# Kernel optimization log

Hardware: AMD Instinct MI355X
Metric: run time of the kernel (lower is better)

## Reference

```python
import jax, jax.numpy as jnp
import numpy as np

NEG_INF_DIAG = 1000000.0

def setup_inputs() -> dict:
    key = jax.random.key(0)
    k1, k2, k3 = jax.random.split(key, 3)
    B, N, S, D = 64, 32, 256, 128
    return {
        "query_embeddings": jax.random.normal(k1, (B, N, D), dtype=jnp.float32),
        "doc_embeddings": jax.random.normal(k2, (B, S, D), dtype=jnp.float32),
        "neg_doc_embeddings": jax.random.normal(k3, (B, S, D), dtype=jnp.float32),
    }

def _maxsim(q, d):
    # q: (b, n, dim), d: (b, s, dim) -> (b,) sum over n of max over s of q.d
    return jnp.einsum('bnd,bsd->bns', q, d).max(axis=2).sum(axis=1)

def reference(query_embeddings, doc_embeddings, neg_doc_embeddings):
    pos_scores = _maxsim(query_embeddings, doc_embeddings)
    neg_scores = _maxsim(query_embeddings, neg_doc_embeddings)
    loss = jax.nn.softplus(neg_scores - pos_scores).mean()

    # in-batch term: scores[b, c] = MaxSim(query b, doc c)
    scores = jnp.einsum('bnd,csd->bcns', query_embeddings, doc_embeddings).max(axis=3).sum(axis=2)  # (B, B)
    pos = jnp.diagonal(scores)
    B = scores.shape[0]
    neg = (scores - jnp.eye(B, dtype=scores.dtype) * NEG_INF_DIAG).max(axis=1)
    loss = loss + jax.nn.softplus(neg - pos).mean()
    return loss / 2
```

## Files before the change

kernel.cpp:

```cpp
#include <hip/hip_runtime.h>
#include <hip/hip_bf16.h>

#define B_SZ 64
#define N_Q 32

typedef __attribute__((ext_vector_type(8))) short bf16x8;
typedef __attribute__((ext_vector_type(4))) float f32x4;

static __device__ __forceinline__ unsigned short f2bf(float f) {
    __hip_bfloat16 h = __float2bfloat16(f);
    return *reinterpret_cast<unsigned short*>(&h);
}

static __device__ __forceinline__ bf16x8 cvt_frag(const float* __restrict__ src) {
    float4 a = reinterpret_cast<const float4*>(src)[0];
    float4 b = reinterpret_cast<const float4*>(src)[1];
    union { bf16x8 v; unsigned short u[8]; } t;
    t.u[0] = f2bf(a.x); t.u[1] = f2bf(a.y); t.u[2] = f2bf(a.z); t.u[3] = f2bf(a.w);
    t.u[4] = f2bf(b.x); t.u[5] = f2bf(b.y); t.u[6] = f2bf(b.z); t.u[7] = f2bf(b.w);
    return t.v;
}

#define MFMA(A, Bv, C) __builtin_amdgcn_mfma_f32_16x16x32_bf16(A, Bv, C, 0, 0, 0)

__global__ __launch_bounds__(256) void cvt_permute(const float* __restrict__ q,
                                                   const float* __restrict__ dd,
                                                   const float* __restrict__ nd,
                                                   unsigned short* __restrict__ DP,
                                                   unsigned short* __restrict__ QP) {
    const int blk = blockIdx.x, tid = threadIdx.x;
    if (blk < 2048) {
        const int o = blk * 256 + tid;
        const int doc = o >> 12;
        const int u = o & 4095;
        const int ln = u & 63, nt = (u >> 6) & 3, kk = (u >> 8) & 3, w = u >> 10;
        const int s  = w * 64 + nt * 16 + (ln & 15);
        const int k0 = kk * 32 + (ln >> 4) * 8;
        const float* src = ((doc < 64) ? (dd + (size_t)doc * 32768)
                                       : (nd + (size_t)(doc - 64) * 32768)) + s * 128 + k0;
        reinterpret_cast<bf16x8*>(DP)[o] = cvt_frag(src);
    } else {
        const int g = (blk - 2048) * 256 + tid;
        const int b = g >> 9, u = g & 511;
        const int ln = u & 63, mt = (u >> 6) & 1, kk = u >> 7;
        const int n  = mt * 16 + (ln & 15);
        const int k0 = kk * 32 + (ln >> 4) * 8;
        reinterpret_cast<bf16x8*>(QP)[g] = cvt_frag(q + (size_t)b * 4096 + n * 128 + k0);
    }
}

__global__ __launch_bounds__(256, 2) void maxsim_kernel(const unsigned short* __restrict__ QP,
                                                        const unsigned short* __restrict__ DP,
                                                        float* __restrict__ scores) {
    const int idx = blockIdx.x;
    int b0, nb, ccol, dcc;
    if (idx < 1024) {
        dcc = idx >> 4; b0 = (idx & 15) * 4; nb = 4; ccol = dcc;
    } else {
        b0 = idx - 1024; nb = 1; ccol = B_SZ; dcc = B_SZ + b0;
    }

    const int tid = threadIdx.x;
    const int wave = tid >> 6, lane = tid & 63;
    const int l15 = lane & 15, l4 = lane >> 4;

    __shared__ bf16x8 docB[4][16][64];
    __shared__ float wred[4][4][N_Q];

    const bf16x8* dsrc = reinterpret_cast<const bf16x8*>(DP)
                         + (size_t)dcc * 4096 + wave * 1024 + lane;
    #pragma unroll
    for (int f = 0; f < 16; ++f)
        docB[wave][f][lane] = dsrc[f * 64];

    const bf16x8* QP8 = reinterpret_cast<const bf16x8*>(QP);

    const int npairs = (nb + 1) >> 1;
    for (int g = 0; g < npairs; ++g) {
        const int bb0 = 2 * g;
        const int bb1 = (2 * g + 1 < nb) ? 2 * g + 1 : 2 * g;
        const bf16x8* qA = QP8 + (size_t)(b0 + bb0) * 512 + lane;
        const bf16x8* qB = QP8 + (size_t)(b0 + bb1) * 512 + lane;

        f32x4 acc[2][2][4] = {};
        #pragma unroll
        for (int kk = 0; kk < 4; ++kk) {
            bf16x8 aA0 = qA[kk * 128];
            bf16x8 aA1 = qA[kk * 128 + 64];
            bf16x8 aB0 = qB[kk * 128];
            bf16x8 aB1 = qB[kk * 128 + 64];
            #pragma unroll
            for (int nt = 0; nt < 4; ++nt) {
                bf16x8 Bv = docB[wave][kk * 4 + nt][lane];
                acc[0][0][nt] = MFMA(aA0, Bv, acc[0][0][nt]);
                acc[0][1][nt] = MFMA(aA1, Bv, acc[0][1][nt]);
                acc[1][0][nt] = MFMA(aB0, Bv, acc[1][0][nt]);
                acc[1][1][nt] = MFMA(aB1, Bv, acc[1][1][nt]);
            }
        }

        #pragma unroll
        for (int h = 0; h < 2; ++h) {
            const int bb = (h == 0) ? bb0 : bb1;
            #pragma unroll
            for (int mt = 0; mt < 2; ++mt) {
                #pragma unroll
                for (int reg = 0; reg < 4; ++reg) {
                    float m = fmaxf(fmaxf(acc[h][mt][0][reg], acc[h][mt][1][reg]),
                                    fmaxf(acc[h][mt][2][reg], acc[h][mt][3][reg]));
                    m = fmaxf(m, __shfl_xor(m, 1, 64));
                    m = fmaxf(m, __shfl_xor(m, 2, 64));
                    m = fmaxf(m, __shfl_xor(m, 4, 64));
                    m = fmaxf(m, __shfl_xor(m, 8, 64));
                    if (l15 == 0) wred[bb][wave][mt * 16 + l4 * 4 + reg] = m;
                }
            }
        }
    }
    __syncthreads();

    const int bb = tid >> 5;
    const int n  = tid & 31;
    if (bb < nb) {
        float m = fmaxf(fmaxf(wred[bb][0][n], wred[bb][1][n]),
                        fmaxf(wred[bb][2][n], wred[bb][3][n]));
        m += __shfl_xor(m, 1, 64);
        m += __shfl_xor(m, 2, 64);
        m += __shfl_xor(m, 4, 64);
        m += __shfl_xor(m, 8, 64);
        m += __shfl_xor(m, 16, 64);
        if (n == 0) scores[(size_t)(b0 + bb) * 65 + ccol] = m;
    }
}

static __device__ __forceinline__ float softplusf(float x) {
    return fmaxf(x, 0.0f) + log1pf(expf(-fabsf(x)));
}

__global__ __launch_bounds__(64) void loss_kernel(const float* __restrict__ scores,
                                                  float* __restrict__ out) {
    const int b = threadIdx.x;
    const float* row = scores + b * 65;
    const float pos  = row[b];
    const float negq = row[64];
    float nib = -1e30f;
    #pragma unroll
    for (int c = 0; c < B_SZ; ++c) {
        float v = row[c] - ((c == b) ? 1000000.0f : 0.0f);
        nib = fmaxf(nib, v);
    }
    float t = softplusf(negq - pos) + softplusf(nib - pos);
    t += __shfl_xor(t, 1, 64);
    t += __shfl_xor(t, 2, 64);
    t += __shfl_xor(t, 4, 64);
    t += __shfl_xor(t, 8, 64);
    t += __shfl_xor(t, 16, 64);
    t += __shfl_xor(t, 32, 64);
    if (b == 0) out[0] = t * (0.5f / 64.0f);
}

extern "C" void kernel_launch(void* const* d_in, const int* in_sizes, int n_in,
                              void* d_out, int out_size, void* d_ws, size_t ws_size,
                              hipStream_t stream) {
    const float* q  = (const float*)d_in[0];
    const float* dd = (const float*)d_in[1];
    const float* nd = (const float*)d_in[2];
    float* out = (float*)d_out;

    unsigned short* DP = (unsigned short*)d_ws;
    unsigned short* QP = DP + (size_t)128 * 32768;
    float* scores = (float*)(QP + (size_t)64 * 4096);

    cvt_permute<<<2176, 256, 0, stream>>>(q, dd, nd, DP, QP);

    maxsim_kernel<<<1024 + B_SZ, 256, 0, stream>>>(QP, DP, scores);

    loss_kernel<<<1, 64, 0, stream>>>(scores, out);
}
```

Measured before the change: 100.7 us.

## Give each wave its own query across all doc chunks, keeping Q fragments in registers

```diff
diff --git a/kernel.cpp b/kernel.cpp
--- a/kernel.cpp
+++ b/kernel.cpp
@@ -33,8 +33,8 @@
         const int o = blk * 256 + tid;
         const int doc = o >> 12;
         const int u = o & 4095;
-        const int ln = u & 63, nt = (u >> 6) & 3, kk = (u >> 8) & 3, w = u >> 10;
-        const int s  = w * 64 + nt * 16 + (ln & 15);
+        const int ln = u & 63, nt = (u >> 6) & 3, kk = (u >> 8) & 3, ch = u >> 10;
+        const int s  = ch * 64 + nt * 16 + (ln & 15);
         const int k0 = kk * 32 + (ln >> 4) * 8;
         const float* src = ((doc < 64) ? (dd + (size_t)doc * 32768)
                                        : (nd + (size_t)(doc - 64) * 32768)) + s * 128 + k0;
@@ -52,84 +52,98 @@
 __global__ __launch_bounds__(256, 2) void maxsim_kernel(const unsigned short* __restrict__ QP,
                                                         const unsigned short* __restrict__ DP,
                                                         float* __restrict__ scores) {
-    const int idx = blockIdx.x;
-    int b0, nb, ccol, dcc;
-    if (idx < 1024) {
-        dcc = idx >> 4; b0 = (idx & 15) * 4; nb = 4; ccol = dcc;
-    } else {
-        b0 = idx - 1024; nb = 1; ccol = B_SZ; dcc = B_SZ + b0;
+    const int wg  = blockIdx.x;
+    const int tid = threadIdx.x;
+    const int wave = tid >> 6, lane = tid & 63;
+    const int l15 = lane & 15;
+
+    __shared__ bf16x8 docB[4096];
+    __shared__ float wredN[4][4][8];
+
+    const bf16x8* DP8 = reinterpret_cast<const bf16x8*>(DP);
+    const bf16x8* QP8 = reinterpret_cast<const bf16x8*>(QP);
+
+    int c, b;
+    bool isNeg;
+    if (wg < 1024) { c = wg >> 4; b = (wg & 15) * 4 + wave; isNeg = false; }
+    else           { b = wg - 1024; c = b; isNeg = true; }
+    const int dcc = isNeg ? (64 + b) : c;
+
+    bf16x8 Af[4][2];
+    const bf16x8* qsrc = QP8 + (size_t)b * 512 + lane;
+    #pragma unroll
+    for (int kk = 0; kk < 4; ++kk) {
+        Af[kk][0] = qsrc[kk * 128];
+        Af[kk][1] = qsrc[kk * 128 + 64];
     }
 
-    const int tid = threadIdx.x;
-    const int wave = tid >> 6, lane = tid & 63;
-    const int l15 = lane & 15, l4 = lane >> 4;
-
-    __shared__ bf16x8 docB[4][16][64];
-    __shared__ float wred[4][4][N_Q];
-
-    const bf16x8* dsrc = reinterpret_cast<const bf16x8*>(DP)
-                         + (size_t)dcc * 4096 + wave * 1024 + lane;
+    const bf16x8* dsrc = DP8 + (size_t)dcc * 4096 + wave * 1024 + lane;
     #pragma unroll
     for (int f = 0; f < 16; ++f)
-        docB[wave][f][lane] = dsrc[f * 64];
+        docB[wave * 1024 + f * 64 + lane] = dsrc[f * 64];
+    __syncthreads();
 
-    const bf16x8* QP8 = reinterpret_cast<const bf16x8*>(QP);
+    float rmax[2][4];
+    #pragma unroll
+    for (int mt = 0; mt < 2; ++mt)
+        #pragma unroll
+        for (int r = 0; r < 4; ++r) rmax[mt][r] = -3.0e38f;
 
-    const int npairs = (nb + 1) >> 1;
-    for (int g = 0; g < npairs; ++g) {
-        const int bb0 = 2 * g;
-        const int bb1 = (2 * g + 1 < nb) ? 2 * g + 1 : 2 * g;
-        const bf16x8* qA = QP8 + (size_t)(b0 + bb0) * 512 + lane;
-        const bf16x8* qB = QP8 + (size_t)(b0 + bb1) * 512 + lane;
-
-        f32x4 acc[2][2][4] = {};
+    const int nch = isNeg ? 1 : 4;
+    for (int i = 0; i < nch; ++i) {
+        const int ch = isNeg ? wave : ((wave + i) & 3);
+        f32x4 acc[2][4] = {};
         #pragma unroll
         for (int kk = 0; kk < 4; ++kk) {
-            bf16x8 aA0 = qA[kk * 128];
-            bf16x8 aA1 = qA[kk * 128 + 64];
-            bf16x8 aB0 = qB[kk * 128];
-            bf16x8 aB1 = qB[kk * 128 + 64];
             #pragma unroll
             for (int nt = 0; nt < 4; ++nt) {
-                bf16x8 Bv = docB[wave][kk * 4 + nt][lane];
-                acc[0][0][nt] = MFMA(aA0, Bv, acc[0][0][nt]);
-                acc[0][1][nt] = MFMA(aA1, Bv, acc[0][1][nt]);
-                acc[1][0][nt] = MFMA(aB0, Bv, acc[1][0][nt]);
-                acc[1][1][nt] = MFMA(aB1, Bv, acc[1][1][nt]);
+                bf16x8 Bv = docB[ch * 1024 + kk * 256 + nt * 64 + lane];
+                acc[0][nt] = MFMA(Af[kk][0], Bv, acc[0][nt]);
+                acc[1][nt] = MFMA(Af[kk][1], Bv, acc[1][nt]);
             }
         }
+        #pragma unroll
+        for (int mt = 0; mt < 2; ++mt)
+            #pragma unroll
+            for (int r = 0; r < 4; ++r)
+                rmax[mt][r] = fmaxf(rmax[mt][r],
+                    fmaxf(fmaxf(acc[mt][0][r], acc[mt][1][r]),
+                          fmaxf(acc[mt][2][r], acc[mt][3][r])));
+    }
 
+    float part = 0.0f;
+    #pragma unroll
+    for (int mt = 0; mt < 2; ++mt)
         #pragma unroll
-        for (int h = 0; h < 2; ++h) {
-            const int bb = (h == 0) ? bb0 : bb1;
-            #pragma unroll
-            for (int mt = 0; mt < 2; ++mt) {
-                #pragma unroll
-                for (int reg = 0; reg < 4; ++reg) {
-                    float m = fmaxf(fmaxf(acc[h][mt][0][reg], acc[h][mt][1][reg]),
-                                    fmaxf(acc[h][mt][2][reg], acc[h][mt][3][reg]));
-                    m = fmaxf(m, __shfl_xor(m, 1, 64));
-                    m = fmaxf(m, __shfl_xor(m, 2, 64));
-                    m = fmaxf(m, __shfl_xor(m, 4, 64));
-                    m = fmaxf(m, __shfl_xor(m, 8, 64));
-                    if (l15 == 0) wred[bb][wave][mt * 16 + l4 * 4 + reg] = m;
-                }
+        for (int r = 0; r < 4; ++r) {
+            float m = rmax[mt][r];
+            m = fmaxf(m, __shfl_xor(m, 1, 64));
+            m = fmaxf(m, __shfl_xor(m, 2, 64));
+            m = fmaxf(m, __shfl_xor(m, 4, 64));
+            m = fmaxf(m, __shfl_xor(m, 8, 64));
+            if (isNeg) {
+                if (l15 == 0) wredN[wave][lane >> 4][mt * 4 + r] = m;
+            } else {
+                part += m;
             }
         }
-    }
-    __syncthreads();
-
-    const int bb = tid >> 5;
-    const int n  = tid & 31;
-    if (bb < nb) {
-        float m = fmaxf(fmaxf(wred[bb][0][n], wred[bb][1][n]),
-                        fmaxf(wred[bb][2][n], wred[bb][3][n]));
-        m += __shfl_xor(m, 1, 64);
-        m += __shfl_xor(m, 2, 64);
-        m += __shfl_xor(m, 4, 64);
-        m += __shfl_xor(m, 8, 64);
-        m += __shfl_xor(m, 16, 64);
-        if (n == 0) scores[(size_t)(b0 + bb) * 65 + ccol] = m;
+    if (!isNeg) {
+        part += __shfl_xor(part, 16, 64);
+        part += __shfl_xor(part, 32, 64);
+        if (lane == 0) scores[(size_t)b * 65 + c] = part;
+    } else {
+        __syncthreads();
+        if (tid < 32) {
+            const int l4v = tid >> 3, slot = tid & 7;
+            float m = fmaxf(fmaxf(wredN[0][l4v][slot], wredN[1][l4v][slot]),
+                            fmaxf(wredN[2][l4v][slot], wredN[3][l4v][slot]));
+            m += __shfl_xor(m, 1, 64);
+            m += __shfl_xor(m, 2, 64);
+            m += __shfl_xor(m, 4, 64);
+            m += __shfl_xor(m, 8, 64);
+            m += __shfl_xor(m, 16, 64);
+            if (tid == 0) scores[(size_t)b * 65 + 64] = m;
+        }
     }
 }
 
```

Measured after the change: 88.18 us. 12.4% less time.
